# Performance work log

Measured on AMD Instinct MI355X. Metric: run time of the kernel, lower is better.

## Reference

```python
import jax, jax.numpy as jnp
import numpy as np

D = 384; QK = 48; E = 768; LOCAL = E - D
NB = 8; NTOK = 100; NEG = -1e30
B = 128; S = 100; NPTS = 256


def layernorm(x, w, eps=1e-5):
    mu = jnp.mean(x, axis=-1, keepdims=True)
    var = jnp.mean((x - mu) ** 2, axis=-1, keepdims=True)
    return (x - mu) * jax.lax.rsqrt(var + eps) * w


def attend(q, k, v, bias=None):
    scale = 1.0 / jnp.sqrt(jnp.asarray(q.shape[-1], q.dtype))
    s = jnp.einsum('bqd,bkd->bqk', q, k) * scale
    if bias is not None:
        s = s + bias
    return jnp.einsum('bqk,bkd->bqd', jax.nn.softmax(s, axis=-1), v)


def setup_inputs() -> dict:
    key = jax.random.key(0)
    ks = jax.random.split(key, 16)
    s_exp = 0.5 / (D ** 0.5) / 2.0   # 0.5 / sqrt(residual_depth) / expand_factor
    s_prj = 1.0 / (D ** 0.5) / 2.0 / NB
    return {
        'q': jax.random.randint(ks[0], (B, S), 0, NTOK),
        'pts': jax.random.randint(ks[1], (B, NPTS, 2), 0, NTOK),
        'emb': jax.random.normal(ks[2], (NTOK, D), jnp.float32),
        'pt_emb': jax.random.normal(ks[3], (NTOK, D // 2), jnp.float32),
        'norm_w': jnp.ones((D,), jnp.float32),
        'out_w': jax.random.normal(ks[4], (NTOK, D), jnp.float32) / (D ** 0.5),
        'ln1': jnp.ones((NB, D), jnp.float32),
        'expand': s_exp * jax.random.normal(ks[5], (NB, 2 * QK + 2 * E, D), jnp.float32),
        'project1': s_prj * jax.random.normal(ks[6], (NB, D, E), jnp.float32),
        'bias_mult': jnp.ones((NB,), jnp.float32),
        'ln2': jnp.ones((NB, D), jnp.float32),
        'Wq': s_exp * jax.random.normal(ks[7], (NB, QK + 2 * LOCAL, D), jnp.float32),
        'Wkv': s_exp * jax.random.normal(ks[8], (NB, QK + 2 * D, D), jnp.float32),
        'project2': s_prj * jax.random.normal(ks[9], (NB, D, E), jnp.float32),
    }


def _forward(q, pts, emb, pt_emb, norm_w, out_w, ln1, expand, project1, bias_mult, ln2, Wq, Wkv, project2):
    x = emb[q]                                        # [B,S,D]
    kv = pt_emb[pts].reshape(pts.shape[0], -1, D)     # [B,NPTS,D] (pairs of 2D coords fold into D)
    x = layernorm(x, norm_w)

    pos = jnp.arange(x.shape[1])
    pbb = (pos[None, :] - pos[:, None]).astype(x.dtype)  # position bias base (j - i)
    allowed = pos[None, :] <= pos[:, None]                # causal: attend to past + self

    def step(h, p):
        w_ln1, W_e, W_p1, bm, w_ln2, W_q, W_kv, W_p2 = p
        # --- latent self-attention block ---
        bias = jnp.where(allowed, jax.nn.softplus(bm) * pbb, NEG)
        n = layernorm(h, w_ln1)
        proj = n @ W_e.T                                  # [B,S,2*QK+2*E]
        qr = proj[..., :QK]
        kr = proj[..., QK:2 * QK]
        lin = proj[..., 2 * QK:2 * QK + E]
        pre = proj[..., 2 * QK + E:]
        geglu = lin * jax.nn.gelu(pre, approximate=False)
        attn = attend(qr, kr, geglu[..., LOCAL:], bias)
        h = h + jnp.concatenate([geglu[..., :LOCAL], attn], axis=-1) @ W_p1.T
        # --- latent cross-attention block ---
        n = layernorm(h, w_ln2)
        pq = n @ W_q.T                                    # [B,S,QK+2*LOCAL]
        qr2 = pq[..., :QK]
        g_local = pq[..., QK:QK + LOCAL] * jax.nn.gelu(pq[..., QK + LOCAL:], approximate=False)
        pk = kv @ W_kv.T                                  # [B,NPTS,QK+2*D]
        k2 = pk[..., :QK]
        g_val = pk[..., QK:QK + D] * jax.nn.gelu(pk[..., QK + D:], approximate=False)
        attn2 = attend(qr2, k2, g_val)
        h = h + jnp.concatenate([g_local, attn2], axis=-1) @ W_p2.T
        return h, None

    x, _ = jax.lax.scan(step, x, (ln1, expand, project1, bias_mult, ln2, Wq, Wkv, project2))
    x = layernorm(x, norm_w)
    return x @ out_w.T                                    # [B,S,NTOK]


def reference(q, pts, emb, pt_emb, norm_w, out_w, ln1, expand, project1, bias_mult, ln2, Wq, Wkv, project2):
    return _forward(q, pts, emb, pt_emb, norm_w, out_w, ln1, expand, project1, bias_mult, ln2, Wq, Wkv, project2)
```

## Files before the change

### kernel.cpp

```cpp
#include <hip/hip_runtime.h>
#include <hip/hip_bf16.h>
#include <math.h>

#define B_    128
#define S_    100
#define D_    384
#define QK_   48
#define E_    768
#define LOCAL_ 384
#define NB_   8
#define NTOK_ 100
#define NPTS_ 256
#define M_    (B_*S_)

typedef unsigned short ushort;
typedef __attribute__((ext_vector_type(8))) short  bf16x8;
typedef __attribute__((ext_vector_type(8))) unsigned short ushort8v;
typedef __attribute__((ext_vector_type(4))) float  f32x4;

#define MFMA(a,b,c) __builtin_amdgcn_mfma_f32_16x16x32_bf16(a,b,c,0,0,0)

static __device__ __forceinline__ float gelu_f(float x) {
    float y = 1.5957691216057308f * (x + 0.044715f * x * x * x);
    float e = __expf(y);
    float t = 1.0f - 2.0f / (e + 1.0f);
    return 0.5f * x * (1.0f + t);
}
static __device__ __forceinline__ ushort f2b(float f) {
    union { float f; unsigned u; } x; x.f = f;
    unsigned r = x.u + 0x7FFFu + ((x.u >> 16) & 1u);
    return (ushort)(r >> 16);
}
static __device__ __forceinline__ float b2f(ushort u) {
    union { unsigned u; float f; } x; x.u = ((unsigned)u) << 16;
    return x.f;
}

__global__ __launch_bounds__(256)
void ln_rows(const float* __restrict__ X, const float* __restrict__ w,
             ushort* __restrict__ Y, int nrows)
{
    int row = blockIdx.x * 4 + (threadIdx.x >> 6);
    if (row >= nrows) return;
    int lane = threadIdx.x & 63;
    const float* x = X + (size_t)row * D_;
    float v[6]; float s = 0.f;
    #pragma unroll
    for (int t = 0; t < 6; ++t) { v[t] = x[lane + 64*t]; s += v[t]; }
    #pragma unroll
    for (int off = 32; off; off >>= 1) s += __shfl_xor(s, off);
    float mu = s * (1.f/(float)D_);
    float q = 0.f;
    #pragma unroll
    for (int t = 0; t < 6; ++t) { float d = v[t]-mu; q += d*d; }
    #pragma unroll
    for (int off = 32; off; off >>= 1) q += __shfl_xor(q, off);
    float rs = rsqrtf(q * (1.f/(float)D_) + 1e-5f);
    #pragma unroll
    for (int t = 0; t < 6; ++t)
        Y[(size_t)row*D_ + lane + 64*t] = f2b((v[t]-mu)*rs*w[lane + 64*t]);
}

__global__ __launch_bounds__(256)
void x_init(const int* __restrict__ qtok, const float* __restrict__ emb,
            const float* __restrict__ w, float* __restrict__ Y, int nrows)
{
    int row = blockIdx.x * 4 + (threadIdx.x >> 6);
    if (row >= nrows) return;
    int lane = threadIdx.x & 63;
    const float* x = emb + (size_t)qtok[row] * D_;
    float v[6]; float s = 0.f;
    #pragma unroll
    for (int t = 0; t < 6; ++t) { v[t] = x[lane + 64*t]; s += v[t]; }
    #pragma unroll
    for (int off = 32; off; off >>= 1) s += __shfl_xor(s, off);
    float mu = s * (1.f/(float)D_);
    float q = 0.f;
    #pragma unroll
    for (int t = 0; t < 6; ++t) { float d = v[t]-mu; q += d*d; }
    #pragma unroll
    for (int off = 32; off; off >>= 1) q += __shfl_xor(q, off);
    float rs = rsqrtf(q * (1.f/(float)D_) + 1e-5f);
    float* y = Y + (size_t)row * D_;
    #pragma unroll
    for (int t = 0; t < 6; ++t) y[lane + 64*t] = (v[t]-mu)*rs*w[lane + 64*t];
}

#define WE_SZ  (1632*384)
#define P1_SZ  (384*768)
#define WQ_SZ  (816*384)
#define P2_SZ  (384*768)
#define WTOT   (WE_SZ + P1_SZ + WQ_SZ + P2_SZ)

static __device__ __forceinline__ void wsplit(float v, ushort* wh, ushort* wl, size_t o) {
    ushort h = f2b(v);
    wh[o] = h; wl[o] = f2b(v - b2f(h));
}

__global__ __launch_bounds__(256)
void wconv_all_hi(const float* __restrict__ expand, const float* __restrict__ proj1,
                  const float* __restrict__ wq, const float* __restrict__ proj2,
                  ushort* __restrict__ wh)
{
    int i = blockIdx.x*256 + threadIdx.x;
    if (i >= WTOT) return;
    int blk = blockIdx.y;
    float v;
    if (i < WE_SZ) v = expand[(size_t)blk*WE_SZ + i];
    else if (i < WE_SZ+P1_SZ) v = proj1[(size_t)blk*P1_SZ + (i - WE_SZ)];
    else if (i < WE_SZ+P1_SZ+WQ_SZ) v = wq[(size_t)blk*WQ_SZ + (i - WE_SZ - P1_SZ)];
    else v = proj2[(size_t)blk*P2_SZ + (i - WE_SZ - P1_SZ - WQ_SZ)];
    wh[(size_t)blk*WTOT + i] = f2b(v);
}

__global__ __launch_bounds__(256)
void wconv_hi(const float* __restrict__ we, const float* __restrict__ p1,
              const float* __restrict__ wq, const float* __restrict__ p2,
              ushort* __restrict__ wh)
{
    int i = blockIdx.x*256 + threadIdx.x;
    if (i >= WTOT) return;
    float v;
    if (i < WE_SZ) v = we[i];
    else if (i < WE_SZ+P1_SZ) v = p1[i - WE_SZ];
    else if (i < WE_SZ+P1_SZ+WQ_SZ) v = wq[i - WE_SZ - P1_SZ];
    else v = p2[i - WE_SZ - P1_SZ - WQ_SZ];
    wh[i] = f2b(v);
}

__global__ __launch_bounds__(256)
void wconv1(const float* __restrict__ src, int n,
            ushort* __restrict__ wh, ushort* __restrict__ wl)
{
    int i = blockIdx.x*256 + threadIdx.x;
    if (i >= n) return;
    wsplit(src[i], wh, wl, i);
}

__global__ __launch_bounds__(256)
void pconv(const float* __restrict__ src, ushort* __restrict__ dst)
{
    int i = blockIdx.x*256 + threadIdx.x;
    if (i >= 128*192) return;
    int r = i / 192;
    dst[i] = (r < NTOK_) ? f2b(src[i]) : 0;
}

__global__ __launch_bounds__(256)
void mm_bt64(const ushort* __restrict__ A1, int lda1, int K1,
             const ushort* __restrict__ A2, int lda2,
             const ushort* __restrict__ Wgh, const ushort* __restrict__ Wgl,
             float* __restrict__ C, int ldc, int N, int K, int accum)
{
    __shared__ ushort Ah[64][72], Wh[64][72], Wl[64][72];
    int tid = threadIdx.x;
    int row0 = blockIdx.y*64, col0 = blockIdx.x*64;
    int srow = tid >> 3;
    int sseg = (tid & 7) * 8;
    int wid = tid >> 6, lane = tid & 63;
    int wr = wid >> 1, wc = wid & 1;
    int fr = lane & 15, fg = lane >> 4;
    f32x4 acc[2][2] = {};
    for (int k0 = 0; k0 < K; k0 += 64) {
        ushort8v va[2], vc[2], vd[2];
        #pragma unroll
        for (int p = 0; p < 2; ++p) {
            int r = p*32 + srow;
            int arow = row0 + r;
            int wrow = col0 + r;
            int gk = k0 + sseg;
            if (gk < K1) va[p] = *(const ushort8v*)(A1 + (size_t)arow*lda1 + gk);
            else         va[p] = *(const ushort8v*)(A2 + (size_t)arow*lda2 + (gk-K1));
            if (wrow >= N) wrow = N - 1;
            vc[p] = *(const ushort8v*)(Wgh + (size_t)wrow*K + gk);
            vd[p] = *(const ushort8v*)(Wgl + (size_t)wrow*K + gk);
        }
        __syncthreads();
        #pragma unroll
        for (int p = 0; p < 2; ++p) {
            int r = p*32 + srow;
            *(ushort8v*)&Ah[r][sseg] = va[p];
            *(ushort8v*)&Wh[r][sseg] = vc[p];
            *(ushort8v*)&Wl[r][sseg] = vd[p];
        }
        __syncthreads();
        #pragma unroll
        for (int kk = 0; kk < 64; kk += 32) {
            bf16x8 a[2], b_h[2], b_l[2];
            #pragma unroll
            for (int s = 0; s < 2; ++s) {
                a[s]   = *(const bf16x8*)&Ah[wr*32 + s*16 + fr][kk + fg*8];
                b_h[s] = *(const bf16x8*)&Wh[wc*32 + s*16 + fr][kk + fg*8];
                b_l[s] = *(const bf16x8*)&Wl[wc*32 + s*16 + fr][kk + fg*8];
            }
            #pragma unroll
            for (int s = 0; s < 2; ++s)
                #pragma unroll
                for (int u = 0; u < 2; ++u)
                    acc[s][u] = MFMA(a[s], b_h[u], acc[s][u]);
            #pragma unroll
            for (int s = 0; s < 2; ++s)
                #pragma unroll
                for (int u = 0; u < 2; ++u)
                    acc[s][u] = MFMA(a[s], b_l[u], acc[s][u]);
        }
        __syncthreads();
    }
    #pragma unroll
    for (int s = 0; s < 2; ++s) {
        int r = row0 + wr*32 + s*16 + fg*4;
        #pragma unroll
        for (int u = 0; u < 2; ++u) {
            int c = col0 + wc*32 + u*16 + fr;
            if (c < N) {
                #pragma unroll
                for (int j = 0; j < 4; ++j) {
                    size_t o = (size_t)(r+j)*ldc + c;
                    C[o] = accum ? (C[o] + acc[s][u][j]) : acc[s][u][j];
                }
            }
        }
    }
}

__global__ __launch_bounds__(256)
void mm_bt2(const ushort* __restrict__ A1, int lda1, int K1,
            const ushort* __restrict__ A2, int lda2,
            const ushort* __restrict__ Wgh,
            float* __restrict__ C, int ldc, int N, int K, int accum)
{
    __shared__ ushort As[2][128*32], Whs[2][64*32];
    int tid = threadIdx.x;
    int lane = tid & 63, wid = tid >> 6;
    int row0 = blockIdx.y*128, col0 = blockIdx.x*64;
    int wr = wid >> 1, wc = wid & 1;
    int fr = lane & 15, fg = lane >> 4;
    int gsl = (fg ^ ((fr >> 1) & 3)) * 8;
    int sr = tid >> 2, sg0 = tid & 3;
    int g = sg0 ^ ((sr >> 1) & 3);
    int wrow = col0 + sr; if (wrow >= N) wrow = N - 1;

    ushort8v va[2], vh;
    auto loadk = [&](int k0) {
        const ushort* Asrc; int lda, kk;
        if (k0 < K1) { Asrc = A1; lda = lda1; kk = k0; }
        else         { Asrc = A2; lda = lda2; kk = k0 - K1; }
        #pragma unroll
        for (int i = 0; i < 2; ++i)
            va[i] = *(const ushort8v*)(Asrc + (size_t)(row0 + sr + i*64)*lda + kk + g*8);
        vh = *(const ushort8v*)(Wgh + (size_t)wrow*K + k0 + g*8);
    };
    auto store = [&](int buf) {
        #pragma unroll
        for (int i = 0; i < 2; ++i)
            *(ushort8v*)&As[buf][(sr + i*64)*32 + sg0*8] = va[i];
        *(ushort8v*)&Whs[buf][sr*32 + sg0*8] = vh;
    };

    int nsteps = K >> 5;
    f32x4 acc[4][2] = {};
    loadk(0);
    store(0);
    __syncthreads();
    for (int t = 0; t < nsteps; ++t) {
        int buf = t & 1;
        if (t + 1 < nsteps) loadk((t+1)*32);
        bf16x8 a[4], bh[2];
        #pragma unroll
        for (int s = 0; s < 4; ++s) {
            int r = wr*64 + s*16 + fr;
            a[s] = *(const bf16x8*)&As[buf][r*32 + gsl];
        }
        #pragma unroll
        for (int u = 0; u < 2; ++u) {
            int r = wc*32 + u*16 + fr;
            bh[u] = *(const bf16x8*)&Whs[buf][r*32 + gsl];
        }
        #pragma unroll
        for (int s = 0; s < 4; ++s)
            #pragma unroll
            for (int u = 0; u < 2; ++u)
                acc[s][u] = MFMA(a[s], bh[u], acc[s][u]);
        if (t + 1 < nsteps) store(buf ^ 1);
        __syncthreads();
    }
    #pragma unroll
    for (int s = 0; s < 4; ++s) {
        int rb = row0 + wr*64 + s*16 + fg*4;
        #pragma unroll
        for (int u = 0; u < 2; ++u) {
            int c = col0 + wc*32 + u*16 + fr;
            if (c < N) {
                #pragma unroll
                for (int j = 0; j < 4; ++j) {
                    size_t o = (size_t)(rb+j)*ldc + c;
                    C[o] = accum ? (C[o] + acc[s][u][j]) : acc[s][u][j];
                }
            }
        }
    }
}

__global__ __launch_bounds__(256)
void mm_fused2(const ushort* __restrict__ Ag, int lda,
               const ushort* __restrict__ Wqh,
               int Nq, int nqt, float* __restrict__ Qout, int ldq,
               const ushort* __restrict__ W1h, const ushort* __restrict__ W2h,
               ushort* __restrict__ Oh, int ldo, int K)
{
    __shared__ ushort As[2][128*32];
    __shared__ ushort Xs[2][2][64*32];
    int tid = threadIdx.x;
    int lane = tid & 63, wid = tid >> 6;
    int row0 = blockIdx.y*128;
    int wr = wid >> 1, wc = wid & 1;
    int fr = lane & 15, fg = lane >> 4;
    int gsl = (fg ^ ((fr >> 1) & 3)) * 8;
    int sr = tid >> 2, sg0 = tid & 3;
    int g = sg0 ^ ((sr >> 1) & 3);
    int nsteps = K >> 5;

    if ((int)blockIdx.x < nqt) {
        int col0 = blockIdx.x*64;
        int wrow = col0 + sr; if (wrow >= Nq) wrow = Nq - 1;
        ushort8v va[2], vh;
        auto loadk = [&](int k0) {
            #pragma unroll
            for (int i = 0; i < 2; ++i)
                va[i] = *(const ushort8v*)(Ag + (size_t)(row0 + sr + i*64)*lda + k0 + g*8);
            vh = *(const ushort8v*)(Wqh + (size_t)wrow*K + k0 + g*8);
        };
        auto store = [&](int buf) {
            #pragma unroll
            for (int i = 0; i < 2; ++i)
                *(ushort8v*)&As[buf][(sr + i*64)*32 + sg0*8] = va[i];
            *(ushort8v*)&Xs[buf][0][sr*32 + sg0*8] = vh;
        };
        f32x4 acc[4][2] = {};
        loadk(0);
        store(0);
        __syncthreads();
        for (int t = 0; t < nsteps; ++t) {
            int buf = t & 1;
            if (t + 1 < nsteps) loadk((t+1)*32);
            bf16x8 a[4], bh[2];
            #pragma unroll
            for (int s = 0; s < 4; ++s) {
                int r = wr*64 + s*16 + fr;
                a[s] = *(const bf16x8*)&As[buf][r*32 + gsl];
            }
            #pragma unroll
            for (int u = 0; u < 2; ++u) {
                int r = wc*32 + u*16 + fr;
                bh[u] = *(const bf16x8*)&Xs[buf][0][r*32 + gsl];
            }
            #pragma unroll
            for (int s = 0; s < 4; ++s)
                #pragma unroll
                for (int u = 0; u < 2; ++u)
                    acc[s][u] = MFMA(a[s], bh[u], acc[s][u]);
            if (t + 1 < nsteps) store(buf ^ 1);
            __syncthreads();
        }
        #pragma unroll
        for (int s = 0; s < 4; ++s) {
            int rb = row0 + wr*64 + s*16 + fg*4;
            #pragma unroll
            for (int u = 0; u < 2; ++u) {
                int c = col0 + wc*32 + u*16 + fr;
                if (c < Nq) {
                    #pragma unroll
                    for (int j = 0; j < 4; ++j)
                        Qout[(size_t)(rb+j)*ldq + c] = acc[s][u][j];
                }
            }
        }
    } else {
        int col0 = ((int)blockIdx.x - nqt)*64;
        ushort8v va[2], vw0, vw2;
        auto loadk = [&](int k0) {
            #pragma unroll
            for (int i = 0; i < 2; ++i)
                va[i] = *(const ushort8v*)(Ag + (size_t)(row0 + sr + i*64)*lda + k0 + g*8);
            size_t wro = (size_t)(col0 + sr)*K + k0 + g*8;
            vw0 = *(const ushort8v*)(W1h + wro);
            vw2 = *(const ushort8v*)(W2h + wro);
        };
        auto store = [&](int buf) {
            #pragma unroll
            for (int i = 0; i < 2; ++i)
                *(ushort8v*)&As[buf][(sr + i*64)*32 + sg0*8] = va[i];
            int o = sr*32 + sg0*8;
            *(ushort8v*)&Xs[buf][0][o] = vw0;
            *(ushort8v*)&Xs[buf][1][o] = vw2;
        };
        f32x4 acc1[4][2] = {}, acc2[4][2] = {};
        loadk(0);
        store(0);
        __syncthreads();
        for (int t = 0; t < nsteps; ++t) {
            int buf = t & 1;
            if (t + 1 < nsteps) loadk((t+1)*32);
            bf16x8 a[4], b1[2], b2[2];
            #pragma unroll
            for (int s = 0; s < 4; ++s) {
                int r = wr*64 + s*16 + fr;
                a[s] = *(const bf16x8*)&As[buf][r*32 + gsl];
            }
            #pragma unroll
            for (int u = 0; u < 2; ++u) {
                int r = wc*32 + u*16 + fr;
                b1[u] = *(const bf16x8*)&Xs[buf][0][r*32 + gsl];
                b2[u] = *(const bf16x8*)&Xs[buf][1][r*32 + gsl];
            }
            #pragma unroll
            for (int s = 0; s < 4; ++s)
                #pragma unroll
                for (int u = 0; u < 2; ++u) {
                    acc1[s][u] = MFMA(a[s], b1[u], acc1[s][u]);
                    acc2[s][u] = MFMA(a[s], b2[u], acc2[s][u]);
                }
            if (t + 1 < nsteps) store(buf ^ 1);
            __syncthreads();
        }
        #pragma unroll
        for (int s = 0; s < 4; ++s) {
            int rb = row0 + wr*64 + s*16 + fg*4;
            #pragma unroll
            for (int u = 0; u < 2; ++u) {
                int c = col0 + wc*32 + u*16 + fr;
                #pragma unroll
                for (int j = 0; j < 4; ++j) {
                    float gg = acc1[s][u][j] * gelu_f(acc2[s][u][j]);
                    Oh[(size_t)(rb+j)*ldo + c] = f2b(gg);
                }
            }
        }
    }
}

__global__ __launch_bounds__(256)
void pk_mm(const ushort* __restrict__ A,
           const ushort* __restrict__ Wh_, const ushort* __restrict__ Wl_,
           float* __restrict__ P12)
{
    __shared__ ushort Ah[64][72], Wh[64][72], Wl[64][72];
    int tid = threadIdx.x;
    int z = blockIdx.z, blk = z >> 1, half = z & 1;
    int row0 = blockIdx.y*64, col0 = blockIdx.x*64;
    int srow = tid >> 3, sseg = (tid & 7) * 8;
    int wid = tid >> 6, lane = tid & 63;
    int wr = wid >> 1, wc = wid & 1;
    int fr = lane & 15, fg = lane >> 4;
    const ushort* Wbh = Wh_ + (size_t)blk*816*384 + half*192;
    const ushort* Wbl = Wl_ + (size_t)blk*816*384 + half*192;
    float* C = P12 + (size_t)z*128*816;
    f32x4 acc[2][2] = {};
    for (int k0 = 0; k0 < 192; k0 += 64) {
        ushort8v va[2], vc[2], vd[2];
        #pragma unroll
        for (int p = 0; p < 2; ++p) {
            int r = p*32 + srow;
            int wrow = col0 + r; if (wrow >= 816) wrow = 815;
            int gk = k0 + sseg;
            va[p] = *(const ushort8v*)(A + (size_t)(row0 + r)*192 + gk);
            vc[p] = *(const ushort8v*)(Wbh + (size_t)wrow*384 + gk);
            vd[p] = *(const ushort8v*)(Wbl + (size_t)wrow*384 + gk);
        }
        __syncthreads();
        #pragma unroll
        for (int p = 0; p < 2; ++p) {
            int r = p*32 + srow;
            *(ushort8v*)&Ah[r][sseg] = va[p];
            *(ushort8v*)&Wh[r][sseg] = vc[p];
            *(ushort8v*)&Wl[r][sseg] = vd[p];
        }
        __syncthreads();
        #pragma unroll
        for (int kk = 0; kk < 64; kk += 32) {
            bf16x8 a[2], b_h[2], b_l[2];
            #pragma unroll
            for (int s = 0; s < 2; ++s) {
                a[s]   = *(const bf16x8*)&Ah[wr*32 + s*16 + fr][kk + fg*8];
                b_h[s] = *(const bf16x8*)&Wh[wc*32 + s*16 + fr][kk + fg*8];
                b_l[s] = *(const bf16x8*)&Wl[wc*32 + s*16 + fr][kk + fg*8];
            }
            #pragma unroll
            for (int s = 0; s < 2; ++s)
                #pragma unroll
                for (int u = 0; u < 2; ++u)
                    acc[s][u] = MFMA(a[s], b_h[u], acc[s][u]);
            #pragma unroll
            for (int s = 0; s < 2; ++s)
                #pragma unroll
                for (int u = 0; u < 2; ++u)
                    acc[s][u] = MFMA(a[s], b_l[u], acc[s][u]);
        }
        __syncthreads();
    }
    #pragma unroll
    for (int s = 0; s < 2; ++s) {
        int r = row0 + wr*32 + s*16 + fg*4;
        #pragma unroll
        for (int u = 0; u < 2; ++u) {
            int c = col0 + wc*32 + u*16 + fr;
            if (c < 816) {
                #pragma unroll
                for (int j = 0; j < 4; ++j)
                    C[(size_t)(r+j)*816 + c] = acc[s][u][j];
            }
        }
    }
}

__global__ __launch_bounds__(256)
void pv2(const ushort* __restrict__ P, int ldp, long sP,
         const ushort* __restrict__ V, int ldv, long sV,
         ushort* __restrict__ Oh, int ldo, long sO,
         int Mrows, int K, int Kv)
{
    __shared__ ushort Ps[2][64*40];
    __shared__ ushort Vs[2][128*32];
    const ushort* Pb = P + (size_t)blockIdx.z * sP;
    const ushort* Vb = V + (size_t)blockIdx.z * sV;
    ushort* Ohb = Oh + (size_t)blockIdx.z * sO;
    int tid = threadIdx.x;
    int row0 = blockIdx.y*64, col0 = blockIdx.x*128;
    int wid = tid >> 6, lane = tid & 63;
    int fr = lane & 15, fg = lane >> 4;
    int prow = tid >> 2, pseg = (tid & 3) * 8;
    int vk = tid & 31, vcb = (tid >> 5) * 8;

    ushort8v pv_, vv[2];
    auto loadk = [&](int k0) {
        pv_ = (ushort8v){0,0,0,0,0,0,0,0};
        int grow = row0 + prow;
        if (grow < Mrows)
            pv_ = *(const ushort8v*)(Pb + (size_t)grow*ldp + k0 + pseg);
        vv[0] = (ushort8v){0,0,0,0,0,0,0,0};
        vv[1] = (ushort8v){0,0,0,0,0,0,0,0};
        int gk = k0 + vk;
        if (gk < Kv) {
            #pragma unroll
            for (int i = 0; i < 2; ++i)
                vv[i] = *(const ushort8v*)(Vb + (size_t)gk*ldv + col0 + vcb + i*64);
        }
    };
    auto store = [&](int buf) {
        *(ushort8v*)&Ps[buf][prow*40 + pseg] = pv_;
        #pragma unroll
        for (int i = 0; i < 2; ++i) {
            #pragma unroll
            for (int e = 0; e < 8; ++e) {
                int c = vcb + i*64 + e;
                Vs[buf][c*32 + (vk & 7) + 8*((vk >> 3) ^ ((c >> 3) & 3))] = vv[i][e];
            }
        }
    };

    int nsteps = K >> 5;
    f32x4 acc[4][2] = {};
    loadk(0);
    store(0);
    __syncthreads();
    for (int t = 0; t < nsteps; ++t) {
        int buf = t & 1;
        if (t + 1 < nsteps) loadk((t+1)*32);
        bf16x8 a[4], b[2];
        #pragma unroll
        for (int s = 0; s < 4; ++s)
            a[s] = *(const bf16x8*)&Ps[buf][(s*16 + fr)*40 + fg*8];
        #pragma unroll
        for (int u = 0; u < 2; ++u) {
            int c = wid*32 + u*16 + fr;
            b[u] = *(const bf16x8*)&Vs[buf][c*32 + 8*(fg ^ ((c >> 3) & 3))];
        }
        #pragma unroll
        for (int s = 0; s < 4; ++s)
            #pragma unroll
            for (int u = 0; u < 2; ++u)
                acc[s][u] = MFMA(a[s], b[u], acc[s][u]);
        if (t + 1 < nsteps) store(buf ^ 1);
        __syncthreads();
    }
    #pragma unroll
    for (int s = 0; s < 4; ++s) {
        int rbase = row0 + s*16 + fg*4;
        #pragma unroll
        for (int u = 0; u < 2; ++u) {
            int c = col0 + wid*32 + u*16 + fr;
            #pragma unroll
            for (int j = 0; j < 4; ++j) {
                int r = rbase + j;
                if (r < Mrows)
                    Ohb[(size_t)r*ldo + c] = f2b(acc[s][u][j]);
            }
        }
    }
}

__global__ __launch_bounds__(256)
void attn1_score(const float* __restrict__ qk, const float* __restrict__ bm, int blk,
                 ushort* __restrict__ P)
{
    __shared__ float qrs[50][QK_];
    __shared__ float krs[S_][QK_+1];
    int b = blockIdx.x, r0 = blockIdx.y*50;
    int tid = threadIdx.x;
    for (int idx = tid; idx < 50*QK_; idx += 256) {
        int r = idx / QK_, c = idx % QK_;
        qrs[r][c] = qk[((size_t)(b*S_ + r0 + r))*96 + c];
    }
    for (int idx = tid; idx < S_*QK_; idx += 256) {
        int r = idx / QK_, c = idx % QK_;
        krs[r][c] = qk[((size_t)(b*S_ + r))*96 + 48 + c];
    }
    __syncthreads();
    float bmv = bm[blk];
    float sp = (bmv > 20.f) ? bmv : log1pf(expf(bmv));
    const float scale = 0.14433756729740643f;
    int w = tid >> 6, lane = tid & 63;
    for (int t = 0; t < 13; ++t) {
        int li = w + 4*t;
        if (li >= 50) break;
        int i = r0 + li;
        int j1 = lane, j2 = lane + 64;
        float s1 = -1e30f, s2 = -1e30f;
        if (j1 <= i) {
            float acc = 0.f;
            #pragma unroll
            for (int l = 0; l < QK_; ++l) acc += qrs[li][l]*krs[j1][l];
            s1 = acc*scale + sp*(float)(j1 - i);
        }
        if (j2 <= i) {
            float acc = 0.f;
            #pragma unroll
            for (int l = 0; l < QK_; ++l) acc += qrs[li][l]*krs[j2][l];
            s2 = acc*scale + sp*(float)(j2 - i);
        }
        float m = fmaxf(s1, s2);
        #pragma unroll
        for (int off = 32; off; off >>= 1) m = fmaxf(m, __shfl_xor(m, off));
        float p1 = (j1 <= i) ? expf(s1 - m) : 0.f;
        float p2 = (j2 <= i) ? expf(s2 - m) : 0.f;
        float sum = p1 + p2;
        #pragma unroll
        for (int off = 32; off; off >>= 1) sum += __shfl_xor(sum, off);
        float inv = 1.f / sum;
        ushort* prow = P + ((size_t)(b*S_) + i)*128;
        prow[j1] = f2b(p1*inv);
        prow[j2] = f2b(p2*inv);
    }
}

__global__ __launch_bounds__(256)
void attn2_score(const float* __restrict__ q2, const float* __restrict__ k2,
                 ushort* __restrict__ P)
{
    __shared__ float ks[NPTS_][QK_+1];
    int b = blockIdx.x, r0 = blockIdx.y*20;
    int tid = threadIdx.x;
    for (int idx = tid; idx < NPTS_*QK_; idx += 256) {
        int r = idx / QK_, c = idx % QK_;
        ks[r][c] = k2[((size_t)(b*NPTS_ + r))*QK_ + c];
    }
    __syncthreads();
    const float scale = 0.14433756729740643f;
    int w = tid >> 6, lane = tid & 63;
    for (int t = 0; t < 5; ++t) {
        int i = r0 + w + 4*t;
        const float* qr = q2 + ((size_t)(b*S_ + i))*QK_;
        float s[4] = {0.f,0.f,0.f,0.f};
        for (int l = 0; l < QK_; ++l) {
            float ql = qr[l];
            #pragma unroll
            for (int r = 0; r < 4; ++r) s[r] += ql * ks[lane + 64*r][l];
        }
        #pragma unroll
        for (int r = 0; r < 4; ++r) s[r] *= scale;
        float m = fmaxf(fmaxf(s[0],s[1]), fmaxf(s[2],s[3]));
        #pragma unroll
        for (int off = 32; off; off >>= 1) m = fmaxf(m, __shfl_xor(m, off));
        float p[4]; float sum = 0.f;
        #pragma unroll
        for (int r = 0; r < 4; ++r) { p[r] = expf(s[r]-m); sum += p[r]; }
        #pragma unroll
        for (int off = 32; off; off >>= 1) sum += __shfl_xor(sum, off);
        float inv = 1.f / sum;
        ushort* prow = P + ((size_t)(b*S_) + i)*256;
        #pragma unroll
        for (int r = 0; r < 4; ++r) prow[lane + 64*r] = f2b(p[r]*inv);
    }
}

__global__ __launch_bounds__(256)
void pk_gather(const int* __restrict__ pts, const float* __restrict__ P12, int blk,
               float* __restrict__ k2, ushort* __restrict__ gv)
{
    int pair = blockIdx.x*4 + (threadIdx.x >> 6);
    int lane = threadIdx.x & 63;
    const float* P1 = P12 + (size_t)(blk*2 + 0)*128*816;
    const float* P2 = P12 + (size_t)(blk*2 + 1)*128*816;
    int t0 = pts[2*pair], t1 = pts[2*pair+1];
    const float* a = P1 + (size_t)t0*816;
    const float* c = P2 + (size_t)t1*816;
    if (lane < QK_) k2[(size_t)pair*QK_ + lane] = a[lane] + c[lane];
    #pragma unroll
    for (int t = 0; t < 6; ++t) {
        int i = lane + 64*t;
        float lin = a[48 + i] + c[48 + i];
        float pre = a[432 + i] + c[432 + i];
        gv[(size_t)pair*D_ + i] = f2b(lin * gelu_f(pre));
    }
}

extern "C" void kernel_launch(void* const* d_in, const int* in_sizes, int n_in,
                              void* d_out, int out_size, void* d_ws, size_t ws_size,
                              hipStream_t stream)
{
    const int*   qtok  = (const int*)d_in[0];
    const int*   pts   = (const int*)d_in[1];
    const float* emb   = (const float*)d_in[2];
    const float* ptemb = (const float*)d_in[3];
    const float* normw = (const float*)d_in[4];
    const float* outw  = (const float*)d_in[5];
    const float* ln1   = (const float*)d_in[6];
    const float* expand= (const float*)d_in[7];
    const float* proj1 = (const float*)d_in[8];
    const float* bm    = (const float*)d_in[9];
    const float* ln2   = (const float*)d_in[10];
    const float* Wq    = (const float*)d_in[11];
    const float* Wkv   = (const float*)d_in[12];
    const float* proj2 = (const float*)d_in[13];
    float* out = (float*)d_out;

    char* base = (char*)d_ws;
    size_t off = 0;
    auto alloc = [&](size_t bytes){ void* p = base + off; off += (bytes + 255) & ~(size_t)255; return p; };
    float*  h     = (float*) alloc((size_t)M_*D_*4);
    ushort* nh    = (ushort*)alloc((size_t)M_*D_*2);
    float*  qk1   = (float*) alloc((size_t)M_*96*4);
    ushort* gegl  = (ushort*)alloc((size_t)M_*E_*2);
    ushort* atb   = (ushort*)alloc((size_t)M_*D_*2);
    ushort* Pbuf  = (ushort*)alloc((size_t)M_*256*2);
    ushort* gv    = (ushort*)alloc((size_t)B_*NPTS_*D_*2);
    float*  P12   = (float*) alloc((size_t)16*128*816*4);
    float*  k2    = (float*) alloc((size_t)B_*NPTS_*QK_*4);
    ushort* wkvh  = (ushort*)alloc((size_t)NB_*816*384*2);
    ushort* wkvl  = (ushort*)alloc((size_t)NB_*816*384*2);
    ushort* ptp   = (ushort*)alloc((size_t)128*192*2);
    ushort* obh   = (ushort*)alloc((size_t)NTOK_*D_*2);
    ushort* obl   = (ushort*)alloc((size_t)NTOK_*D_*2);

    size_t rem = (ws_size > off) ? (ws_size - off) : 0;
    bool fits8 = rem >= ((size_t)NB_ * WTOT * 2 + 1024);
    int nlay = fits8 ? NB_ : 1;
    ushort* wbh = (ushort*)alloc((size_t)nlay*WTOT*2);
    size_t wstride = fits8 ? (size_t)WTOT : 0;

    float*  qr2   = qk1;
    ushort* gloc  = gegl;

    const size_t oWE = 0;
    const size_t oP1 = WE_SZ;
    const size_t oWQ = WE_SZ + P1_SZ;
    const size_t oP2 = WE_SZ + P1_SZ + WQ_SZ;

    x_init<<<M_/4, 256, 0, stream>>>(qtok, emb, normw, h, M_);
    pconv<<<(128*192 + 255)/256, 256, 0, stream>>>(ptemb, ptp);
    wconv1<<<(NB_*816*384 + 255)/256, 256, 0, stream>>>(Wkv, NB_*816*384, wkvh, wkvl);
    pk_mm<<<dim3(13, 2, 16), 256, 0, stream>>>(ptp, wkvh, wkvl, P12);
    if (fits8)
        wconv_all_hi<<<dim3((WTOT+255)/256, NB_), 256, 0, stream>>>(
            expand, proj1, Wq, proj2, wbh);

    for (int blk = 0; blk < NB_; ++blk) {
        if (!fits8)
            wconv_hi<<<(WTOT+255)/256, 256, 0, stream>>>(
                expand + (size_t)blk*WE_SZ, proj1 + (size_t)blk*P1_SZ,
                Wq + (size_t)blk*WQ_SZ, proj2 + (size_t)blk*P2_SZ, wbh);
        const ushort* Lh = wbh + wstride*blk;

        ln_rows<<<M_/4, 256, 0, stream>>>(h, ln1 + blk*D_, nh, M_);
        mm_fused2<<<dim3(14, M_/128), 256, 0, stream>>>(nh, D_,
            Lh + oWE, 96, 2, qk1, 96,
            Lh + oWE + (size_t)96*D_, Lh + oWE + (size_t)864*D_,
            gegl, E_, D_);
        attn1_score<<<dim3(B_,2), 256, 0, stream>>>(qk1, bm, blk, Pbuf);
        pv2<<<dim3(3,2,B_), 256, 0, stream>>>(Pbuf, 128, (long)S_*128,
            gegl + LOCAL_, E_, (long)S_*E_,
            atb, D_, (long)S_*D_, S_, 128, S_);
        mm_bt2<<<dim3(6, M_/128), 256, 0, stream>>>(gegl, E_, D_, atb, D_,
            Lh + oP1, h, D_, D_, E_, 1);

        ln_rows<<<M_/4, 256, 0, stream>>>(h, ln2 + blk*D_, nh, M_);
        mm_fused2<<<dim3(7, M_/128), 256, 0, stream>>>(nh, D_,
            Lh + oWQ, 48, 1, qr2, 48,
            Lh + oWQ + (size_t)48*D_, Lh + oWQ + (size_t)432*D_,
            gloc, D_, D_);
        pk_gather<<<B_*NPTS_/4, 256, 0, stream>>>(pts, P12, blk, k2, gv);
        attn2_score<<<dim3(B_,5), 256, 0, stream>>>(qr2, k2, Pbuf);
        pv2<<<dim3(3,2,B_), 256, 0, stream>>>(Pbuf, 256, (long)S_*256,
            gv, D_, (long)NPTS_*D_,
            atb, D_, (long)S_*D_, S_, 256, 256);
        mm_bt2<<<dim3(6, M_/128), 256, 0, stream>>>(gloc, D_, D_, atb, D_,
            Lh + oP2, h, D_, D_, E_, 1);
    }

    ln_rows<<<M_/4, 256, 0, stream>>>(h, normw, nh, M_);
    wconv1<<<(NTOK_*D_ + 255)/256, 256, 0, stream>>>(outw, NTOK_*D_, obh, obl);
    mm_bt64<<<dim3(2, M_/64), 256, 0, stream>>>(nh, D_, D_, nh, D_,
        obh, obl, out, NTOK_, NTOK_, D_, 0);
}
```

Before: 1.814 ms.

## Load A-operand fragments directly from global into registers, skipping LDS staging

Three GEMM kernels (mm_bt2, mm_fused2, pv2) no longer stage the A (activation/probability) tiles through shared memory. Each wave now loads its own MFMA fragments straight from global memory into registers, and the loop is unrolled by two with register ping-pong buffers. Only the weight/V tiles still go through LDS. This removes LDS traffic and shared-memory footprint, but loses the coalesced cooperative loads: each row is now read by both column-waves, and loads are strided 16-byte per-lane accesses that may be less efficient from L2.

```diff
diff --git a/kernel.cpp b/kernel.cpp
--- a/kernel.cpp
+++ b/kernel.cpp
@@ -229,7 +229,7 @@
             const ushort* __restrict__ Wgh,
             float* __restrict__ C, int ldc, int N, int K, int accum)
 {
-    __shared__ ushort As[2][128*32], Whs[2][64*32];
+    __shared__ ushort Whs[2][64*32];
     int tid = threadIdx.x;
     int lane = tid & 63, wid = tid >> 6;
     int row0 = blockIdx.y*128, col0 = blockIdx.x*64;
@@ -240,37 +240,25 @@
     int g = sg0 ^ ((sr >> 1) & 3);
     int wrow = col0 + sr; if (wrow >= N) wrow = N - 1;
 
-    ushort8v va[2], vh;
-    auto loadk = [&](int k0) {
+    ushort8v vh;
+    auto loadW = [&](int k0) {
+        vh = *(const ushort8v*)(Wgh + (size_t)wrow*K + k0 + g*8);
+    };
+    auto storeW = [&](int buf) {
+        *(ushort8v*)&Whs[buf][sr*32 + sg0*8] = vh;
+    };
+    bf16x8 aA[4], aB[4];
+    auto loadA = [&](int k0, bf16x8* a) {
         const ushort* Asrc; int lda, kk;
         if (k0 < K1) { Asrc = A1; lda = lda1; kk = k0; }
         else         { Asrc = A2; lda = lda2; kk = k0 - K1; }
         #pragma unroll
-        for (int i = 0; i < 2; ++i)
-            va[i] = *(const ushort8v*)(Asrc + (size_t)(row0 + sr + i*64)*lda + kk + g*8);
-        vh = *(const ushort8v*)(Wgh + (size_t)wrow*K + k0 + g*8);
+        for (int s = 0; s < 4; ++s)
+            a[s] = *(const bf16x8*)(Asrc + (size_t)(row0 + wr*64 + s*16 + fr)*lda + kk + fg*8);
     };
-    auto store = [&](int buf) {
-        #pragma unroll
-        for (int i = 0; i < 2; ++i)
-            *(ushort8v*)&As[buf][(sr + i*64)*32 + sg0*8] = va[i];
-        *(ushort8v*)&Whs[buf][sr*32 + sg0*8] = vh;
-    };
-
-    int nsteps = K >> 5;
     f32x4 acc[4][2] = {};
-    loadk(0);
-    store(0);
-    __syncthreads();
-    for (int t = 0; t < nsteps; ++t) {
-        int buf = t & 1;
-        if (t + 1 < nsteps) loadk((t+1)*32);
-        bf16x8 a[4], bh[2];
-        #pragma unroll
-        for (int s = 0; s < 4; ++s) {
-            int r = wr*64 + s*16 + fr;
-            a[s] = *(const bf16x8*)&As[buf][r*32 + gsl];
-        }
+    auto compute = [&](bf16x8* a, int buf) {
+        bf16x8 bh[2];
         #pragma unroll
         for (int u = 0; u < 2; ++u) {
             int r = wc*32 + u*16 + fr;
@@ -281,8 +269,24 @@
             #pragma unroll
             for (int u = 0; u < 2; ++u)
                 acc[s][u] = MFMA(a[s], bh[u], acc[s][u]);
-        if (t + 1 < nsteps) store(buf ^ 1);
-        __syncthreads();
+    };
+
+    int nsteps = K >> 5;
+    loadA(0, aA); loadW(0); storeW(0);
+    __syncthreads();
+    for (int t = 0; t < nsteps; t += 2) {
+        bool h1 = (t + 1 < nsteps);
+        if (h1) { loadA((t+1)*32, aB); loadW((t+1)*32); }
+        compute(aA, 0);
+        if (h1) storeW(1);
+        __syncthreads();
+        if (h1) {
+            bool h2 = (t + 2 < nsteps);
+            if (h2) { loadA((t+2)*32, aA); loadW((t+2)*32); }
+            compute(aB, 1);
+            if (h2) storeW(0);
+            __syncthreads();
+        }
     }
     #pragma unroll
     for (int s = 0; s < 4; ++s) {
@@ -308,7 +312,6 @@
                const ushort* __restrict__ W1h, const ushort* __restrict__ W2h,
                ushort* __restrict__ Oh, int ldo, int K)
 {
-    __shared__ ushort As[2][128*32];
     __shared__ ushort Xs[2][2][64*32];
     int tid = threadIdx.x;
     int lane = tid & 63, wid = tid >> 6;
@@ -320,35 +323,26 @@
     int g = sg0 ^ ((sr >> 1) & 3);
     int nsteps = K >> 5;
 
+    bf16x8 aA[4], aB[4];
+    auto loadA = [&](int k0, bf16x8* a) {
+        #pragma unroll
+        for (int s = 0; s < 4; ++s)
+            a[s] = *(const bf16x8*)(Ag + (size_t)(row0 + wr*64 + s*16 + fr)*lda + k0 + fg*8);
+    };
+
     if ((int)blockIdx.x < nqt) {
         int col0 = blockIdx.x*64;
         int wrow = col0 + sr; if (wrow >= Nq) wrow = Nq - 1;
-        ushort8v va[2], vh;
-        auto loadk = [&](int k0) {
-            #pragma unroll
-            for (int i = 0; i < 2; ++i)
-                va[i] = *(const ushort8v*)(Ag + (size_t)(row0 + sr + i*64)*lda + k0 + g*8);
+        ushort8v vh;
+        auto loadW = [&](int k0) {
             vh = *(const ushort8v*)(Wqh + (size_t)wrow*K + k0 + g*8);
         };
-        auto store = [&](int buf) {
-            #pragma unroll
-            for (int i = 0; i < 2; ++i)
-                *(ushort8v*)&As[buf][(sr + i*64)*32 + sg0*8] = va[i];
+        auto storeW = [&](int buf) {
             *(ushort8v*)&Xs[buf][0][sr*32 + sg0*8] = vh;
         };
         f32x4 acc[4][2] = {};
-        loadk(0);
-        store(0);
-        __syncthreads();
-        for (int t = 0; t < nsteps; ++t) {
-            int buf = t & 1;
-            if (t + 1 < nsteps) loadk((t+1)*32);
-            bf16x8 a[4], bh[2];
-            #pragma unroll
-            for (int s = 0; s < 4; ++s) {
-                int r = wr*64 + s*16 + fr;
-                a[s] = *(const bf16x8*)&As[buf][r*32 + gsl];
-            }
+        auto compute = [&](bf16x8* a, int buf) {
+            bf16x8 bh[2];
             #pragma unroll
             for (int u = 0; u < 2; ++u) {
                 int r = wc*32 + u*16 + fr;
@@ -359,8 +353,22 @@
                 #pragma unroll
                 for (int u = 0; u < 2; ++u)
                     acc[s][u] = MFMA(a[s], bh[u], acc[s][u]);
-            if (t + 1 < nsteps) store(buf ^ 1);
+        };
+        loadA(0, aA); loadW(0); storeW(0);
+        __syncthreads();
+        for (int t = 0; t < nsteps; t += 2) {
+            bool h1 = (t + 1 < nsteps);
+            if (h1) { loadA((t+1)*32, aB); loadW((t+1)*32); }
+            compute(aA, 0);
+            if (h1) storeW(1);
             __syncthreads();
+            if (h1) {
+                bool h2 = (t + 2 < nsteps);
+                if (h2) { loadA((t+2)*32, aA); loadW((t+2)*32); }
+                compute(aB, 1);
+                if (h2) storeW(0);
+                __syncthreads();
+            }
         }
         #pragma unroll
         for (int s = 0; s < 4; ++s) {
@@ -377,36 +385,20 @@
         }
     } else {
         int col0 = ((int)blockIdx.x - nqt)*64;
-        ushort8v va[2], vw0, vw2;
-        auto loadk = [&](int k0) {
-            #pragma unroll
-            for (int i = 0; i < 2; ++i)
-                va[i] = *(const ushort8v*)(Ag + (size_t)(row0 + sr + i*64)*lda + k0 + g*8);
+        ushort8v vw0, vw2;
+        auto loadW = [&](int k0) {
             size_t wro = (size_t)(col0 + sr)*K + k0 + g*8;
             vw0 = *(const ushort8v*)(W1h + wro);
             vw2 = *(const ushort8v*)(W2h + wro);
         };
-        auto store = [&](int buf) {
-            #pragma unroll
-            for (int i = 0; i < 2; ++i)
-                *(ushort8v*)&As[buf][(sr + i*64)*32 + sg0*8] = va[i];
+        auto storeW = [&](int buf) {
             int o = sr*32 + sg0*8;
             *(ushort8v*)&Xs[buf][0][o] = vw0;
             *(ushort8v*)&Xs[buf][1][o] = vw2;
         };
         f32x4 acc1[4][2] = {}, acc2[4][2] = {};
-        loadk(0);
-        store(0);
-        __syncthreads();
-        for (int t = 0; t < nsteps; ++t) {
-            int buf = t & 1;
-            if (t + 1 < nsteps) loadk((t+1)*32);
-            bf16x8 a[4], b1[2], b2[2];
-            #pragma unroll
-            for (int s = 0; s < 4; ++s) {
-                int r = wr*64 + s*16 + fr;
-                a[s] = *(const bf16x8*)&As[buf][r*32 + gsl];
-            }
+        auto compute = [&](bf16x8* a, int buf) {
+            bf16x8 b1[2], b2[2];
             #pragma unroll
             for (int u = 0; u < 2; ++u) {
                 int r = wc*32 + u*16 + fr;
@@ -420,8 +412,22 @@
                     acc1[s][u] = MFMA(a[s], b1[u], acc1[s][u]);
                     acc2[s][u] = MFMA(a[s], b2[u], acc2[s][u]);
                 }
-            if (t + 1 < nsteps) store(buf ^ 1);
+        };
+        loadA(0, aA); loadW(0); storeW(0);
+        __syncthreads();
+        for (int t = 0; t < nsteps; t += 2) {
+            bool h1 = (t + 1 < nsteps);
+            if (h1) { loadA((t+1)*32, aB); loadW((t+1)*32); }
+            compute(aA, 0);
+            if (h1) storeW(1);
             __syncthreads();
+            if (h1) {
+                bool h2 = (t + 2 < nsteps);
+                if (h2) { loadA((t+2)*32, aA); loadW((t+2)*32); }
+                compute(aB, 1);
+                if (h2) storeW(0);
+                __syncthreads();
+            }
         }
         #pragma unroll
         for (int s = 0; s < 4; ++s) {
@@ -519,7 +525,6 @@
          ushort* __restrict__ Oh, int ldo, long sO,
          int Mrows, int K, int Kv)
 {
-    __shared__ ushort Ps[2][64*40];
     __shared__ ushort Vs[2][128*32];
     const ushort* Pb = P + (size_t)blockIdx.z * sP;
     const ushort* Vb = V + (size_t)blockIdx.z * sV;
@@ -528,15 +533,20 @@
     int row0 = blockIdx.y*64, col0 = blockIdx.x*128;
     int wid = tid >> 6, lane = tid & 63;
     int fr = lane & 15, fg = lane >> 4;
-    int prow = tid >> 2, pseg = (tid & 3) * 8;
     int vk = tid & 31, vcb = (tid >> 5) * 8;
 
-    ushort8v pv_, vv[2];
-    auto loadk = [&](int k0) {
-        pv_ = (ushort8v){0,0,0,0,0,0,0,0};
-        int grow = row0 + prow;
-        if (grow < Mrows)
-            pv_ = *(const ushort8v*)(Pb + (size_t)grow*ldp + k0 + pseg);
+    const ushort* pr0; const ushort* pr1; const ushort* pr2; const ushort* pr3;
+    {
+        int r0 = row0 + 0*16 + fr; if (r0 >= Mrows) r0 = Mrows - 1;
+        int r1 = row0 + 1*16 + fr; if (r1 >= Mrows) r1 = Mrows - 1;
+        int r2 = row0 + 2*16 + fr; if (r2 >= Mrows) r2 = Mrows - 1;
+        int r3 = row0 + 3*16 + fr; if (r3 >= Mrows) r3 = Mrows - 1;
+        pr0 = Pb + (size_t)r0*ldp; pr1 = Pb + (size_t)r1*ldp;
+        pr2 = Pb + (size_t)r2*ldp; pr3 = Pb + (size_t)r3*ldp;
+    }
+
+    ushort8v vv[2];
+    auto loadV = [&](int k0) {
         vv[0] = (ushort8v){0,0,0,0,0,0,0,0};
         vv[1] = (ushort8v){0,0,0,0,0,0,0,0};
         int gk = k0 + vk;
@@ -546,8 +556,7 @@
                 vv[i] = *(const ushort8v*)(Vb + (size_t)gk*ldv + col0 + vcb + i*64);
         }
     };
-    auto store = [&](int buf) {
-        *(ushort8v*)&Ps[buf][prow*40 + pseg] = pv_;
+    auto storeV = [&](int buf) {
         #pragma unroll
         for (int i = 0; i < 2; ++i) {
             #pragma unroll
@@ -557,19 +566,16 @@
             }
         }
     };
-
-    int nsteps = K >> 5;
+    bf16x8 aA[4], aB[4];
+    auto loadP = [&](int k0, bf16x8* a) {
+        a[0] = *(const bf16x8*)(pr0 + k0 + fg*8);
+        a[1] = *(const bf16x8*)(pr1 + k0 + fg*8);
+        a[2] = *(const bf16x8*)(pr2 + k0 + fg*8);
+        a[3] = *(const bf16x8*)(pr3 + k0 + fg*8);
+    };
     f32x4 acc[4][2] = {};
-    loadk(0);
-    store(0);
-    __syncthreads();
-    for (int t = 0; t < nsteps; ++t) {
-        int buf = t & 1;
-        if (t + 1 < nsteps) loadk((t+1)*32);
-        bf16x8 a[4], b[2];
-        #pragma unroll
-        for (int s = 0; s < 4; ++s)
-            a[s] = *(const bf16x8*)&Ps[buf][(s*16 + fr)*40 + fg*8];
+    auto compute = [&](bf16x8* a, int buf) {
+        bf16x8 b[2];
         #pragma unroll
         for (int u = 0; u < 2; ++u) {
             int c = wid*32 + u*16 + fr;
@@ -580,8 +586,24 @@
             #pragma unroll
             for (int u = 0; u < 2; ++u)
                 acc[s][u] = MFMA(a[s], b[u], acc[s][u]);
-        if (t + 1 < nsteps) store(buf ^ 1);
-        __syncthreads();
+    };
+
+    int nsteps = K >> 5;
+    loadP(0, aA); loadV(0); storeV(0);
+    __syncthreads();
+    for (int t = 0; t < nsteps; t += 2) {
+        bool h1 = (t + 1 < nsteps);
+        if (h1) { loadP((t+1)*32, aB); loadV((t+1)*32); }
+        compute(aA, 0);
+        if (h1) storeV(1);
+        __syncthreads();
+        if (h1) {
+            bool h2 = (t + 2 < nsteps);
+            if (h2) { loadP((t+2)*32, aA); loadV((t+2)*32); }
+            compute(aB, 1);
+            if (h2) storeV(0);
+            __syncthreads();
+        }
     }
     #pragma unroll
     for (int s = 0; s < 4; ++s) {
```

After: 2.363 ms. 30.3% more time.
